# Kernel optimization log

Hardware: AMD Instinct MI355X
Metric: run time of the kernel (lower is better)

Reference implementation:

```python
import jax, jax.numpy as jnp
import numpy as np
from jax import lax

# --- tree geometry (matches init_kwargs) ---
B_CHAIN = 16384      # backbone length (generation-0 scan path, excluding root)
S_SIDE = 15          # side-chain length per backbone atom (generation-1 scans)
NATM = 1 + B_CHAIN + B_CHAIN * S_SIDE   # 262145, node 0 is the virtual root
N_SEL_PER = 4        # masked DOFs per non-root node (phi_p, theta, d, phi_c)


def _rx(a):
    c, s = jnp.cos(a), jnp.sin(a)
    z, o = jnp.zeros_like(a), jnp.ones_like(a)
    return jnp.stack([jnp.stack([o, z, z, z], -1),
                      jnp.stack([z, c, -s, z], -1),
                      jnp.stack([z, s, c, z], -1),
                      jnp.stack([z, z, z, o], -1)], -2)


def _ry(a):
    c, s = jnp.cos(a), jnp.sin(a)
    z, o = jnp.zeros_like(a), jnp.ones_like(a)
    return jnp.stack([jnp.stack([c, z, s, z], -1),
                      jnp.stack([z, o, z, z], -1),
                      jnp.stack([-s, z, c, z], -1),
                      jnp.stack([z, z, z, o], -1)], -2)


def _rz(a):
    c, s = jnp.cos(a), jnp.sin(a)
    z, o = jnp.zeros_like(a), jnp.ones_like(a)
    return jnp.stack([jnp.stack([c, -s, z, z], -1),
                      jnp.stack([s, c, z, z], -1),
                      jnp.stack([z, z, o, z], -1),
                      jnp.stack([z, z, z, o], -1)], -2)


def _t(x, y, z):
    zz, o = jnp.zeros_like(x), jnp.ones_like(x)
    return jnp.stack([jnp.stack([o, zz, zz, x], -1),
                      jnp.stack([zz, o, zz, y], -1),
                      jnp.stack([zz, zz, o, z], -1),
                      jnp.stack([zz, zz, zz, o], -1)], -2)


def _mm(a, b):
    return jnp.einsum('...ij,...jk->...ik', a, b)


def setup_inputs() -> dict:
    key = jax.random.key(0)
    k_dofs, = jax.random.split(key, 1)
    rng = np.random.default_rng(0)

    # DOF mask: the 4 bond DOFs of every non-root node (selected_dofs)
    node_idx = np.repeat(np.arange(1, NATM, dtype=np.int32), N_SEL_PER)
    dof_idx = np.tile(np.arange(N_SEL_PER, dtype=np.int32), NATM - 1)

    # doftype: 0=root, 1=jump (first backbone node), 2=bond
    doftype = np.full(NATM, 2, dtype=np.int32)
    doftype[0] = 0
    doftype[1] = 1

    # generation-0 scan: root + backbone chain (parent[i] = i-1)
    gen0_nodes = np.arange(B_CHAIN + 1, dtype=np.int32)
    # generation-1 scans: one side-chain path per backbone node
    gen1_nodes = np.arange(1 + B_CHAIN, NATM, dtype=np.int32).reshape(B_CHAIN, S_SIDE)
    gen1_parents = np.arange(1, B_CHAIN + 1, dtype=np.int32)  # parent of each scan's first node

    # kintree.id: id[0] = -1 (root unused), id[1:] a permutation of system indices
    kin_id = np.empty(NATM, dtype=np.int32)
    kin_id[0] = -1
    kin_id[1:] = rng.permutation(NATM - 1).astype(np.int32)

    dofs = 0.5 * jax.random.normal(k_dofs, (N_SEL_PER * (NATM - 1),), dtype=jnp.float32)
    full_dofs = jnp.zeros((NATM, 9), dtype=jnp.float32)

    return {
        'dofs': dofs,
        'full_dofs': full_dofs,
        'node_idx': jnp.asarray(node_idx),
        'dof_idx': jnp.asarray(dof_idx),
        'doftype': jnp.asarray(doftype),
        'gen0_nodes': jnp.asarray(gen0_nodes),
        'gen1_nodes': jnp.asarray(gen1_nodes),
        'gen1_parents': jnp.asarray(gen1_parents),
        'kin_id': jnp.asarray(kin_id),
    }


def reference(dofs, full_dofs, node_idx, dof_idx, doftype, gen0_nodes,
              gen1_nodes, gen1_parents, kin_id):
    natm = full_dofs.shape[0]

    # --- DOFMaskingFunc: scatter selected dofs into the background dofs ---
    full = full_dofs.at[node_idx, dof_idx].set(dofs)

    # --- per-node local homogeneous transforms from dofs ---
    # bond: Rx(phi_p) . Rz(theta) . Tx(d) . Rx(phi_c)
    zero = jnp.zeros_like(full[:, 0])
    ht_bond = _mm(_mm(_rx(full[:, 0]), _rz(full[:, 1])),
                  _mm(_t(full[:, 2], zero, zero), _rx(full[:, 3])))
    # jump: T(x,y,z) . Rz(g) . Ry(b) . Rx(a)
    ht_jump = _mm(_t(full[:, 0], full[:, 1], full[:, 2]),
                  _mm(_rz(full[:, 5]), _mm(_ry(full[:, 4]), _rx(full[:, 3]))))
    dt = doftype[:, None, None]
    eye = jnp.broadcast_to(jnp.eye(4, dtype=full.dtype), (natm, 4, 4))
    ht = jnp.where(dt == 2, ht_bond, jnp.where(dt == 1, ht_jump, eye))

    # --- generation-ordered forward-kinematics scan ---
    # gen 0: single long path starting at root; global[k] = M0 @ ... @ Mk
    g0 = lax.associative_scan(_mm, ht[gen0_nodes], axis=0)
    ht_global = jnp.zeros((natm, 4, 4), dtype=full.dtype).at[gen0_nodes].set(g0)

    # gen 1: independent paths; seed each with its parent's global transform
    ms = ht[gen1_nodes]                                   # [n_scans, S, 4, 4]
    ms = ms.at[:, 0].set(_mm(ht_global[gen1_parents], ms[:, 0]))
    g1 = lax.associative_scan(_mm, ms, axis=1)
    ht_global = ht_global.at[gen1_nodes.reshape(-1)].set(g1.reshape(-1, 4, 4))

    kincoords = ht_global[:, :3, 3]                       # [natm, 3]

    # --- KinematicOperation: scatter kin coords into system coords by id ---
    coords = jnp.full((natm - 1, 3), jnp.nan, dtype=kincoords.dtype)
    coords = coords.at[kin_id[1:]].set(kincoords[1:])
    return coords[None, ...]
```

## Files before the change

kernel.cpp:

```cpp
#include <hip/hip_runtime.h>
#include <math.h>


#define B_CHAIN 16384
#define S_SIDE 15
#define NATM (1 + B_CHAIN + B_CHAIN * S_SIDE)
#define NODES_PER_LANE 4
#define NODES_PER_CHUNK 256
#define NCHUNK 64

struct Aff { float m[12]; };

__device__ __forceinline__ Aff aff_id() {
    Aff a;
    a.m[0]=1.f; a.m[1]=0.f; a.m[2]=0.f;  a.m[3]=0.f;
    a.m[4]=0.f; a.m[5]=1.f; a.m[6]=0.f;  a.m[7]=0.f;
    a.m[8]=0.f; a.m[9]=0.f; a.m[10]=1.f; a.m[11]=0.f;
    return a;
}

__device__ __forceinline__ Aff aff_mul(const Aff& A, const Aff& B) {
    Aff C;
#pragma unroll
    for (int r = 0; r < 3; ++r) {
        const float a0 = A.m[r*4+0], a1 = A.m[r*4+1], a2 = A.m[r*4+2];
#pragma unroll
        for (int c = 0; c < 3; ++c)
            C.m[r*4+c] = a0*B.m[0*4+c] + a1*B.m[1*4+c] + a2*B.m[2*4+c];
        C.m[r*4+3] = a0*B.m[3] + a1*B.m[7] + a2*B.m[11] + A.m[r*4+3];
    }
    return C;
}

__device__ __forceinline__ Aff bond_ht(float a, float b, float x, float cang) {
    float sa, ca, sb, cb, sc, cc;
    sincosf(a, &sa, &ca);
    sincosf(b, &sb, &cb);
    sincosf(cang, &sc, &cc);
    Aff M;
    M.m[0] = cb;      M.m[1] = -sb*cc;            M.m[2] = sb*sc;             M.m[3]  = cb*x;
    M.m[4] = ca*sb;   M.m[5] = ca*cb*cc - sa*sc;  M.m[6] = -ca*cb*sc - sa*cc; M.m[7]  = ca*sb*x;
    M.m[8] = sa*sb;   M.m[9] = sa*cb*cc + ca*sc;  M.m[10]= -sa*cb*sc + ca*cc; M.m[11] = sa*sb*x;
    return M;
}

__device__ __forceinline__ Aff node_ht(int n, const float* __restrict__ dofs) {
    const float4 d = *reinterpret_cast<const float4*>(dofs + 4*(n-1));
    if (n == 1) {
        float s, c; sincosf(d.w, &s, &c);
        Aff M = aff_id();
        M.m[3] = d.x; M.m[7] = d.y; M.m[11] = d.z;
        M.m[5] = c; M.m[6] = -s; M.m[9] = s; M.m[10] = c;
        return M;
    }
    return bond_ht(d.x, d.y, d.z, d.w);
}

__device__ __forceinline__ Aff aff_shfl_up(const Aff& v, int delta, int width) {
    Aff r;
#pragma unroll
    for (int i = 0; i < 12; ++i) r.m[i] = __shfl_up(v.m[i], delta, width);
    return r;
}

__device__ __forceinline__ void aff_store(float* p, const Aff& f) {
    float4* q = reinterpret_cast<float4*>(p);
    q[0] = make_float4(f.m[0], f.m[1], f.m[2],  f.m[3]);
    q[1] = make_float4(f.m[4], f.m[5], f.m[6],  f.m[7]);
    q[2] = make_float4(f.m[8], f.m[9], f.m[10], f.m[11]);
}

__device__ __forceinline__ Aff aff_load(const float* p) {
    const float4* q = reinterpret_cast<const float4*>(p);
    float4 r0 = q[0], r1 = q[1], r2 = q[2];
    Aff f;
    f.m[0]=r0.x; f.m[1]=r0.y; f.m[2]=r0.z;  f.m[3]=r0.w;
    f.m[4]=r1.x; f.m[5]=r1.y; f.m[6]=r1.z;  f.m[7]=r1.w;
    f.m[8]=r2.x; f.m[9]=r2.y; f.m[10]=r2.z; f.m[11]=r2.w;
    return f;
}

__global__ __launch_bounds__(64) void k_scan_local(const float* __restrict__ dofs,
                                                   float* __restrict__ gbuf,
                                                   float* __restrict__ totals) {
    const int lane = threadIdx.x;
    const int chunk = blockIdx.x;
    const int base = 1 + chunk * NODES_PER_CHUNK + lane * NODES_PER_LANE;

    Aff pref[NODES_PER_LANE];
    Aff acc;
#pragma unroll
    for (int j = 0; j < NODES_PER_LANE; ++j) {
        Aff m = node_ht(base + j, dofs);
        acc = (j == 0) ? m : aff_mul(acc, m);
        pref[j] = acc;
    }

    Aff incl = acc;
#pragma unroll
    for (int s = 1; s < 64; s <<= 1) {
        Aff up = aff_shfl_up(incl, s, 64);
        if (lane >= s) incl = aff_mul(up, incl);
    }
    Aff excl = aff_shfl_up(incl, 1, 64);
    const bool have_excl = (lane > 0);

#pragma unroll
    for (int j = 0; j < NODES_PER_LANE; ++j) {
        Aff f = have_excl ? aff_mul(excl, pref[j]) : pref[j];
        aff_store(gbuf + (base + j - 1) * 12, f);
    }
    if (lane == 63) aff_store(totals + chunk * 12, incl);
}

__global__ __launch_bounds__(256) void k_finalize(const float* __restrict__ dofs,
                                                  const int* __restrict__ kin_id,
                                                  const float* __restrict__ gbuf,
                                                  const float* __restrict__ totals,
                                                  float* __restrict__ out) {
    __shared__ float s_tot[NCHUNK * 12];

    if (threadIdx.x < 64) {
        const int lane = threadIdx.x;
        Aff v = aff_load(totals + lane * 12);
#pragma unroll
        for (int s = 1; s < 64; s <<= 1) {
            Aff up = aff_shfl_up(v, s, 64);
            if (lane >= s) v = aff_mul(up, v);
        }
#pragma unroll
        for (int i = 0; i < 12; ++i) s_tot[lane * 12 + i] = v.m[i];
    }
    __syncthreads();

    const int t = blockIdx.x * 256 + threadIdx.x;
    const int c  = t >> 4;
    const int ls = t & 15;
    const int p  = c + 1;

    Aff V;
    int idx;
    if (ls == 0) {
        V = aff_load(gbuf + (p - 1) * 12);
        const int chunk = (p - 1) >> 8;
        if (chunk > 0) {
            Aff pre;
#pragma unroll
            for (int i = 0; i < 12; ++i) pre.m[i] = s_tot[(chunk - 1) * 12 + i];
            V = aff_mul(pre, V);
        }
        idx = p;
    } else {
        const int atom = 1 + B_CHAIN + c * S_SIDE + (ls - 1);
        const float4 d = *reinterpret_cast<const float4*>(dofs + 4*(atom-1));
        V = bond_ht(d.x, d.y, d.z, d.w);
        idx = atom;
    }

#pragma unroll
    for (int s = 1; s < 16; s <<= 1) {
        Aff up = aff_shfl_up(V, s, 16);
        if (ls >= s) V = aff_mul(up, V);
    }

    const int kid = kin_id[idx];
    out[3*kid+0] = V.m[3];
    out[3*kid+1] = V.m[7];
    out[3*kid+2] = V.m[11];
}

extern "C" void kernel_launch(void* const* d_in, const int* in_sizes, int n_in,
                              void* d_out, int out_size, void* d_ws, size_t ws_size,
                              hipStream_t stream) {
    const float* dofs   = (const float*)d_in[0];
    const int*   kin_id = (const int*)  d_in[8];
    float* ws = (float*)d_ws;
    float* gbuf   = ws;
    float* totals = ws + B_CHAIN * 12;

    k_scan_local<<<NCHUNK, 64, 0, stream>>>(dofs, gbuf, totals);
    k_finalize  <<<(B_CHAIN * 16) / 256, 256, 0, stream>>>(dofs, kin_id, gbuf, totals,
                                                           (float*)d_out);
}
```

Measured before the change: 92.01 us.

## Process four side-chain nodes per thread in finalize scan

```diff
diff --git a/kernel.cpp b/kernel.cpp
--- a/kernel.cpp
+++ b/kernel.cpp
@@ -133,40 +133,55 @@
     }
     __syncthreads();
 
-    const int t = blockIdx.x * 256 + threadIdx.x;
-    const int c  = t >> 4;
-    const int ls = t & 15;
-    const int p  = c + 1;
+    const int t   = blockIdx.x * 256 + threadIdx.x;
+    const int c   = t >> 2;
+    const int sub = t & 3;
+    const int p   = c + 1;
 
-    Aff V;
-    int idx;
-    if (ls == 0) {
-        V = aff_load(gbuf + (p - 1) * 12);
-        const int chunk = (p - 1) >> 8;
-        if (chunk > 0) {
-            Aff pre;
+    Aff M[4];
 #pragma unroll
-            for (int i = 0; i < 12; ++i) pre.m[i] = s_tot[(chunk - 1) * 12 + i];
-            V = aff_mul(pre, V);
+    for (int j = 0; j < 4; ++j) {
+        const int k = sub * 4 + j;
+        if (k == 0) {
+            Aff G = aff_load(gbuf + (p - 1) * 12);
+            const int chunk = (p - 1) >> 8;
+            if (chunk > 0) {
+                Aff pre;
+#pragma unroll
+                for (int i = 0; i < 12; ++i) pre.m[i] = s_tot[(chunk - 1) * 12 + i];
+                G = aff_mul(pre, G);
+            }
+            M[j] = G;
+        } else {
+            const int atom = 1 + B_CHAIN + c * S_SIDE + (k - 1);
+            const float4 d = *reinterpret_cast<const float4*>(dofs + 4*(atom-1));
+            M[j] = bond_ht(d.x, d.y, d.z, d.w);
         }
-        idx = p;
-    } else {
-        const int atom = 1 + B_CHAIN + c * S_SIDE + (ls - 1);
-        const float4 d = *reinterpret_cast<const float4*>(dofs + 4*(atom-1));
-        V = bond_ht(d.x, d.y, d.z, d.w);
-        idx = atom;
     }
 
+    Aff P[4];
+    P[0] = M[0];
 #pragma unroll
-    for (int s = 1; s < 16; s <<= 1) {
-        Aff up = aff_shfl_up(V, s, 16);
-        if (ls >= s) V = aff_mul(up, V);
+    for (int j = 1; j < 4; ++j) P[j] = aff_mul(P[j-1], M[j]);
+
+    Aff incl = P[3];
+#pragma unroll
+    for (int s = 1; s < 4; s <<= 1) {
+        Aff up = aff_shfl_up(incl, s, 4);
+        if (sub >= s) incl = aff_mul(up, incl);
     }
+    Aff excl = aff_shfl_up(incl, 1, 4);
 
-    const int kid = kin_id[idx];
-    out[3*kid+0] = V.m[3];
-    out[3*kid+1] = V.m[7];
-    out[3*kid+2] = V.m[11];
+#pragma unroll
+    for (int j = 0; j < 4; ++j) {
+        Aff G = (sub > 0) ? aff_mul(excl, P[j]) : P[j];
+        const int k = sub * 4 + j;
+        const int idx = (k == 0) ? p : (1 + B_CHAIN + c * S_SIDE + (k - 1));
+        const int kid = kin_id[idx];
+        out[3*kid+0] = G.m[3];
+        out[3*kid+1] = G.m[7];
+        out[3*kid+2] = G.m[11];
+    }
 }
 
 extern "C" void kernel_launch(void* const* d_in, const int* in_sizes, int n_in,
@@ -179,6 +194,6 @@
     float* totals = ws + B_CHAIN * 12;
 
     k_scan_local<<<NCHUNK, 64, 0, stream>>>(dofs, gbuf, totals);
-    k_finalize  <<<(B_CHAIN * 16) / 256, 256, 0, stream>>>(dofs, kin_id, gbuf, totals,
-                                                           (float*)d_out);
+    k_finalize  <<<(B_CHAIN * 4) / 256, 256, 0, stream>>>(dofs, kin_id, gbuf, totals,
+                                                          (float*)d_out);
 }
```

After: 92.10 us. Within noise of the previous version (+0.1%).
